# Optimization experiments

Hardware: AMD Instinct MI355X
Metric: run time of the kernel (lower is better)

The kernel has to match this reference:

```python
import jax, jax.numpy as jnp
import numpy as np

N_NODES = 100000
N_EDGES = 3200000
D_IN = 128
D_OUT = 128
EPS = 0.0  # GINConv default eps, not trained


def setup_inputs() -> dict:
    key = jax.random.key(0)
    k1, k2, k3, k4, k5, k6, k7 = jax.random.split(key, 7)
    x = jax.random.normal(k1, (N_NODES, D_IN), dtype=jnp.float32)
    edge_index = jax.random.randint(k2, (2, N_EDGES), 0, N_NODES, dtype=jnp.int64)
    # MLP params: Linear(D_IN->D_OUT), ReLU, Linear(D_OUT->D_OUT)
    s1 = 1.0 / np.sqrt(D_IN)
    s2 = 1.0 / np.sqrt(D_OUT)
    W1 = jax.random.uniform(k3, (D_IN, D_OUT), jnp.float32, -s1, s1)
    b1 = jax.random.uniform(k4, (D_OUT,), jnp.float32, -s1, s1)
    W2 = jax.random.uniform(k5, (D_OUT, D_OUT), jnp.float32, -s2, s2)
    b2 = jax.random.uniform(k6, (D_OUT,), jnp.float32, -s2, s2)
    return {"x": x, "edge_index": edge_index, "W1": W1, "b1": b1, "W2": W2, "b2": b2}


def reference(x, edge_index, W1, b1, W2, b2):
    src, dst = edge_index[0], edge_index[1]
    # message = x[src]; aggregate by sum onto dst (source_to_target flow)
    agg = jax.ops.segment_sum(x[src], dst, num_segments=x.shape[0])  # [N, D_IN]
    h = (1.0 + EPS) * x + agg
    h = jax.nn.relu(h @ W1 + b1)
    return h @ W2 + b2
```

## Files before the change

### kernel.cpp

```cpp
#include <hip/hip_runtime.h>

#define D 128
#define TILE_ROWS 64
#define MLP_THREADS 512
#define SCAN_THREADS 1024
#define BK_NODES 128
#define MAX_BKT 1024
#define EPB 16
#define SC_THREADS 512
#define SC_EPB 24
#define CAPL 6144
#define FMLP_THREADS 512
#define MLP_BM 128
#define HSTR 136

typedef unsigned short ushort_t;
typedef unsigned int uint_t;
typedef __attribute__((ext_vector_type(8))) short short8v;
typedef __attribute__((ext_vector_type(4))) float f32x4;

__device__ __forceinline__ ushort_t f2bf(float f) {
    uint_t u = __float_as_uint(f);
    u = u + 0x7FFFu + ((u >> 16) & 1u);
    return (ushort_t)(u >> 16);
}

__global__ void cast_kernel(const float* __restrict__ x, ushort_t* __restrict__ xh, int n4) {
    int i = blockIdx.x * blockDim.x + threadIdx.x;
    if (i < n4) {
        float4 v = reinterpret_cast<const float4*>(x)[i];
        ushort4 o;
        o.x = f2bf(v.x); o.y = f2bf(v.y); o.z = f2bf(v.z); o.w = f2bf(v.w);
        reinterpret_cast<ushort4*>(xh)[i] = o;
    }
}

__global__ void wprep_kernel(const float* __restrict__ W1, const float* __restrict__ W2,
                             ushort_t* __restrict__ w1t, ushort_t* __restrict__ w2t) {
    int i = blockIdx.x * blockDim.x + threadIdx.x;
    if (i < D * D) {
        int c = i & 127, k = i >> 7;
        w1t[(size_t)c * HSTR + k] = f2bf(W1[(size_t)k * D + c]);
        w2t[(size_t)c * HSTR + k] = f2bf(W2[(size_t)k * D + c]);
    }
}

__global__ void zero_kernel(int* __restrict__ p, int n) {
    int i = blockIdx.x * blockDim.x + threadIdx.x;
    if (i < n) p[i] = 0;
}

__global__ void coarse_hist_kernel(const int* __restrict__ dsts,
                                   int* __restrict__ ghist, int ne, int nbkt) {
    __shared__ int h[MAX_BKT];
    for (int k = threadIdx.x; k < nbkt; k += blockDim.x) h[k] = 0;
    __syncthreads();
    int base = blockIdx.x * blockDim.x * EPB;
    for (int j = 0; j < EPB; ++j) {
        int e = base + j * blockDim.x + threadIdx.x;
        if (e < ne) atomicAdd(&h[dsts[e] >> 7], 1);
    }
    __syncthreads();
    for (int k = threadIdx.x; k < nbkt; k += blockDim.x)
        if (h[k]) atomicAdd(&ghist[k], h[k]);
}

__global__ __launch_bounds__(SCAN_THREADS) void coarse_scan_kernel(
    const int* __restrict__ ghist, int* __restrict__ cbase,
    int* __restrict__ ccursor, int* __restrict__ offsets,
    int nbkt, int nnodes, int ne) {
    __shared__ int sc[SCAN_THREADS];
    int t = threadIdx.x;
    int v = (t < nbkt) ? ghist[t] : 0;
    sc[t] = v;
    __syncthreads();
    for (int off = 1; off < SCAN_THREADS; off <<= 1) {
        int u = (t >= off) ? sc[t - off] : 0;
        __syncthreads();
        sc[t] += u;
        __syncthreads();
    }
    if (t < nbkt) { cbase[t] = sc[t] - v; ccursor[t] = sc[t] - v; }
    if (t == 0) { cbase[nbkt] = sc[SCAN_THREADS - 1]; offsets[nnodes] = ne; }
}

__global__ __launch_bounds__(SC_THREADS) void coarse_scatter_kernel(
    const int* __restrict__ ei, int* __restrict__ ccursor,
    int* __restrict__ pairs, int ne, int nbkt) {
    __shared__ int h[MAX_BKT];
    __shared__ int lbase[MAX_BKT];
    __shared__ int gbase[MAX_BKT];
    __shared__ int lcur[MAX_BKT];
    __shared__ int stot[SC_THREADS];
    __shared__ int stage[SC_THREADS * SC_EPB];

    const int t = threadIdx.x;
    const int base = blockIdx.x * SC_THREADS * SC_EPB;

    for (int k = t; k < MAX_BKT; k += SC_THREADS) h[k] = 0;
    __syncthreads();

    for (int j = 0; j < SC_EPB; ++j) {
        int e = base + j * SC_THREADS + t;
        if (e < ne) atomicAdd(&h[ei[ne + e] >> 7], 1);
    }
    __syncthreads();

    int a0 = h[2 * t], a1 = h[2 * t + 1];
    stot[t] = a0 + a1;
    __syncthreads();
    for (int off = 1; off < SC_THREADS; off <<= 1) {
        int u = (t >= off) ? stot[t - off] : 0;
        __syncthreads();
        stot[t] += u;
        __syncthreads();
    }
    int bexc = stot[t] - (a0 + a1);
    lbase[2 * t] = bexc;
    lbase[2 * t + 1] = bexc + a0;
    lcur[2 * t] = bexc;
    lcur[2 * t + 1] = bexc + a0;
    __syncthreads();

    for (int k = t; k < MAX_BKT; k += SC_THREADS)
        gbase[k] = h[k] ? atomicAdd(&ccursor[k], h[k]) : 0;
    __syncthreads();

    for (int j = 0; j < SC_EPB; ++j) {
        int e = base + j * SC_THREADS + t;
        if (e < ne) {
            int dst = ei[ne + e];
            int src = ei[e];
            int k = dst >> 7;
            int pos = atomicAdd(&lcur[k], 1);
            stage[pos] = (src << 7) | (dst & (BK_NODES - 1));
        }
    }
    __syncthreads();

    const int lane = t & 63, w = t >> 6;
    for (int k = w; k < nbkt; k += (SC_THREADS / 64)) {
        int cnt = h[k];
        int lb = lbase[k], gb = gbase[k];
        for (int i = lane; i < cnt; i += 64)
            pairs[gb + i] = stage[lb + i];
    }
}

__global__ void bucket_csr_kernel(const int* __restrict__ pairs,
                                  const int* __restrict__ cbase,
                                  int* __restrict__ offsets,
                                  int* __restrict__ sorted_src,
                                  int nnodes) {
    __shared__ int h[BK_NODES];
    __shared__ int ex[BK_NODES];
    __shared__ int cur[BK_NODES];
    __shared__ int stage[CAPL];
    int b = blockIdx.x;
    int t = threadIdx.x;
    int rbeg = cbase[b], rend = cbase[b + 1];
    int cnt = rend - rbeg;
    if (t < BK_NODES) h[t] = 0;
    __syncthreads();
    for (int i = rbeg + t; i < rend; i += blockDim.x)
        atomicAdd(&h[pairs[i] & (BK_NODES - 1)], 1);
    __syncthreads();
    if (t < BK_NODES) ex[t] = h[t];
    __syncthreads();
    for (int off = 1; off < BK_NODES; off <<= 1) {
        int u = (t >= off && t < BK_NODES) ? ex[t - off] : 0;
        __syncthreads();
        if (t < BK_NODES) ex[t] += u;
        __syncthreads();
    }
    const bool staged = (cnt <= CAPL);
    if (t < BK_NODES) {
        int e = ex[t] - h[t];
        cur[t] = staged ? e : rbeg + e;
        int node = b * BK_NODES + t;
        if (node < nnodes) offsets[node] = rbeg + e;
    }
    __syncthreads();
    if (staged) {
        for (int i = rbeg + t; i < rend; i += blockDim.x) {
            int p = pairs[i];
            int pos = atomicAdd(&cur[p & (BK_NODES - 1)], 1);
            stage[pos] = p >> 7;
        }
        __syncthreads();
        for (int i = t; i < cnt; i += blockDim.x)
            sorted_src[rbeg + i] = stage[i];
    } else {
        for (int i = rbeg + t; i < rend; i += blockDim.x) {
            int p = pairs[i];
            int pos = atomicAdd(&cur[p & (BK_NODES - 1)], 1);
            sorted_src[pos] = p >> 7;
        }
    }
}

template <int MODE>
__global__ void agg_kernel(const float* __restrict__ x,
                           const ushort_t* __restrict__ xh,
                           const int* __restrict__ sorted_src,
                           const int* __restrict__ offsets,
                           float* __restrict__ out, int nnodes) {
    int gid = blockIdx.x * blockDim.x + threadIdx.x;
    int node = gid >> 6;
    if (node >= nnodes) return;
    int lane = threadIdx.x & 63;
    int beg = offsets[node];
    int end = offsets[node + 1];
    float sx, sy;
    int i = beg;
    if (MODE == 0) {
        const uint_t* xp = reinterpret_cast<const uint_t*>(xh);
        uint_t us = xp[(size_t)node * 64 + lane];
        sx = __uint_as_float(us << 16);
        sy = __uint_as_float(us & 0xffff0000u);
        for (; i + 8 <= end; i += 8) {
            int s0 = sorted_src[i + 0], s1 = sorted_src[i + 1];
            int s2 = sorted_src[i + 2], s3 = sorted_src[i + 3];
            int s4 = sorted_src[i + 4], s5 = sorted_src[i + 5];
            int s6 = sorted_src[i + 6], s7 = sorted_src[i + 7];
            uint_t u0 = xp[(size_t)s0 * 64 + lane];
            uint_t u1 = xp[(size_t)s1 * 64 + lane];
            uint_t u2 = xp[(size_t)s2 * 64 + lane];
            uint_t u3 = xp[(size_t)s3 * 64 + lane];
            uint_t u4 = xp[(size_t)s4 * 64 + lane];
            uint_t u5 = xp[(size_t)s5 * 64 + lane];
            uint_t u6 = xp[(size_t)s6 * 64 + lane];
            uint_t u7 = xp[(size_t)s7 * 64 + lane];
            sx += __uint_as_float(u0 << 16) + __uint_as_float(u1 << 16) +
                  __uint_as_float(u2 << 16) + __uint_as_float(u3 << 16) +
                  __uint_as_float(u4 << 16) + __uint_as_float(u5 << 16) +
                  __uint_as_float(u6 << 16) + __uint_as_float(u7 << 16);
            sy += __uint_as_float(u0 & 0xffff0000u) + __uint_as_float(u1 & 0xffff0000u) +
                  __uint_as_float(u2 & 0xffff0000u) + __uint_as_float(u3 & 0xffff0000u) +
                  __uint_as_float(u4 & 0xffff0000u) + __uint_as_float(u5 & 0xffff0000u) +
                  __uint_as_float(u6 & 0xffff0000u) + __uint_as_float(u7 & 0xffff0000u);
        }
        for (; i < end; ++i) {
            uint_t u = xp[(size_t)sorted_src[i] * 64 + lane];
            sx += __uint_as_float(u << 16);
            sy += __uint_as_float(u & 0xffff0000u);
        }
    } else {
        const float2* xp = reinterpret_cast<const float2*>(x);
        float2 a = xp[(size_t)node * 64 + lane];
        sx = a.x; sy = a.y;
        for (; i + 8 <= end; i += 8) {
            int s0 = sorted_src[i + 0], s1 = sorted_src[i + 1];
            int s2 = sorted_src[i + 2], s3 = sorted_src[i + 3];
            int s4 = sorted_src[i + 4], s5 = sorted_src[i + 5];
            int s6 = sorted_src[i + 6], s7 = sorted_src[i + 7];
            float2 v0 = xp[(size_t)s0 * 64 + lane];
            float2 v1 = xp[(size_t)s1 * 64 + lane];
            float2 v2 = xp[(size_t)s2 * 64 + lane];
            float2 v3 = xp[(size_t)s3 * 64 + lane];
            float2 v4 = xp[(size_t)s4 * 64 + lane];
            float2 v5 = xp[(size_t)s5 * 64 + lane];
            float2 v6 = xp[(size_t)s6 * 64 + lane];
            float2 v7 = xp[(size_t)s7 * 64 + lane];
            sx += ((v0.x + v1.x) + (v2.x + v3.x)) + ((v4.x + v5.x) + (v6.x + v7.x));
            sy += ((v0.y + v1.y) + (v2.y + v3.y)) + ((v4.y + v5.y) + (v6.y + v7.y));
        }
        for (; i < end; ++i) {
            float2 v = xp[(size_t)sorted_src[i] * 64 + lane];
            sx += v.x;
            sy += v.y;
        }
    }
    float2 o;
    o.x = sx;
    o.y = sy;
    reinterpret_cast<float2*>(out)[(size_t)node * 64 + lane] = o;
}

__global__ __launch_bounds__(FMLP_THREADS, 1) void fused_mlp_kernel(
    const float* __restrict__ h, const ushort_t* __restrict__ w1t,
    const ushort_t* __restrict__ w2t, const float* __restrict__ b1,
    const float* __restrict__ b2, float* __restrict__ outp, int nrows) {
    __shared__ ushort_t sh[MLP_BM * HSTR];
    __shared__ ushort_t sw1[D * HSTR];
    __shared__ ushort_t sw2[D * HSTR];
    const int tid = threadIdx.x;
    const int row0 = blockIdx.x * MLP_BM;

    {
        const uint4* s1 = reinterpret_cast<const uint4*>(w1t);
        const uint4* s2 = reinterpret_cast<const uint4*>(w2t);
        uint4* d1 = reinterpret_cast<uint4*>(sw1);
        uint4* d2 = reinterpret_cast<uint4*>(sw2);
        for (int i = tid; i < D * HSTR / 8; i += FMLP_THREADS) { d1[i] = s1[i]; d2[i] = s2[i]; }
    }
    for (int i = tid; i < MLP_BM * 32; i += FMLP_THREADS) {
        int r = i >> 5, c4 = i & 31;
        float4 v = make_float4(0.f, 0.f, 0.f, 0.f);
        if (row0 + r < nrows)
            v = reinterpret_cast<const float4*>(h + (size_t)(row0 + r) * D)[c4];
        ushort4 o;
        o.x = f2bf(v.x); o.y = f2bf(v.y); o.z = f2bf(v.z); o.w = f2bf(v.w);
        *reinterpret_cast<ushort4*>(&sh[r * HSTR + c4 * 4]) = o;
    }
    __syncthreads();

    const int w = tid >> 6, l = tid & 63;
    const int lr = l & 15, lg = l >> 4;
    const int rowb = w * 16;

    short8v A[4];
#pragma unroll
    for (int kk = 0; kk < 4; ++kk)
        A[kk] = *reinterpret_cast<const short8v*>(&sh[(rowb + lr) * HSTR + kk * 32 + lg * 8]);
#pragma unroll
    for (int n = 0; n < 8; ++n) {
        float bv = b1[n * 16 + lr];
        f32x4 acc = {bv, bv, bv, bv};
#pragma unroll
        for (int kk = 0; kk < 4; ++kk) {
            short8v B = *reinterpret_cast<const short8v*>(&sw1[(n * 16 + lr) * HSTR + kk * 32 + lg * 8]);
            acc = __builtin_amdgcn_mfma_f32_16x16x32_bf16(A[kk], B, acc, 0, 0, 0);
        }
#pragma unroll
        for (int r = 0; r < 4; ++r) {
            float v = fmaxf(acc[r], 0.f);
            sh[(rowb + lg * 4 + r) * HSTR + n * 16 + lr] = f2bf(v);
        }
    }

    short8v A2[4];
#pragma unroll
    for (int kk = 0; kk < 4; ++kk)
        A2[kk] = *reinterpret_cast<const short8v*>(&sh[(rowb + lr) * HSTR + kk * 32 + lg * 8]);
#pragma unroll
    for (int n = 0; n < 8; ++n) {
        float bv = b2[n * 16 + lr];
        f32x4 acc = {bv, bv, bv, bv};
#pragma unroll
        for (int kk = 0; kk < 4; ++kk) {
            short8v B = *reinterpret_cast<const short8v*>(&sw2[(n * 16 + lr) * HSTR + kk * 32 + lg * 8]);
            acc = __builtin_amdgcn_mfma_f32_16x16x32_bf16(A2[kk], B, acc, 0, 0, 0);
        }
#pragma unroll
        for (int r = 0; r < 4; ++r) {
            int grow = row0 + rowb + lg * 4 + r;
            if (grow < nrows)
                outp[(size_t)grow * D + n * 16 + lr] = acc[r];
        }
    }
}

__global__ void init_kernel(const float* __restrict__ x, float* __restrict__ out, int n4) {
    int i = blockIdx.x * blockDim.x + threadIdx.x;
    if (i < n4) {
        reinterpret_cast<float4*>(out)[i] = reinterpret_cast<const float4*>(x)[i];
    }
}

__global__ void scatter_kernel(const float* __restrict__ x,
                               const int* __restrict__ ei,
                               float* __restrict__ out, int ne) {
    long long gid = (long long)blockIdx.x * blockDim.x + threadIdx.x;
    int e = (int)(gid >> 5);
    if (e >= ne) return;
    int d0 = ((int)gid & 31) * 4;
    int src = ei[e];
    int dst = ei[ne + e];
    float4 v = *reinterpret_cast<const float4*>(x + (long long)src * D + d0);
    float* o = out + (long long)dst * D + d0;
    atomicAdd(o + 0, v.x);
    atomicAdd(o + 1, v.y);
    atomicAdd(o + 2, v.z);
    atomicAdd(o + 3, v.w);
}

template <bool RELU>
__global__ __launch_bounds__(MLP_THREADS, 1) void mlp_kernel(
    const float* __restrict__ in, const float* __restrict__ W,
    const float* __restrict__ b, float* __restrict__ outp, int nrows) {
    __shared__ float Wl[D][D];
    __shared__ float inl[TILE_ROWS][D + 4];

    const int tid = threadIdx.x;
    const int row0 = blockIdx.x * TILE_ROWS;

    for (int i = tid; i < D * D / 4; i += MLP_THREADS) {
        reinterpret_cast<float4*>(&Wl[0][0])[i] =
            reinterpret_cast<const float4*>(W)[i];
    }
    for (int i = tid; i < TILE_ROWS * (D / 4); i += MLP_THREADS) {
        int r = i >> 5;
        int k4 = i & 31;
        float4 v = make_float4(0.f, 0.f, 0.f, 0.f);
        if (row0 + r < nrows)
            v = *reinterpret_cast<const float4*>(in + (size_t)(row0 + r) * D + 4 * k4);
        *reinterpret_cast<float4*>(&inl[r][4 * k4]) = v;
    }
    __syncthreads();

    const int cg = tid & 31;
    const int rg = tid >> 5;
    const int c0 = cg * 4;
    const int r0 = rg * 4;

    float4 bv = *reinterpret_cast<const float4*>(b + c0);
    float acc[4][4];
#pragma unroll
    for (int i = 0; i < 4; ++i) {
        acc[i][0] = bv.x; acc[i][1] = bv.y; acc[i][2] = bv.z; acc[i][3] = bv.w;
    }

#pragma unroll 4
    for (int k4 = 0; k4 < 32; ++k4) {
        float4 w0 = *reinterpret_cast<const float4*>(&Wl[4 * k4 + 0][c0]);
        float4 w1 = *reinterpret_cast<const float4*>(&Wl[4 * k4 + 1][c0]);
        float4 w2 = *reinterpret_cast<const float4*>(&Wl[4 * k4 + 2][c0]);
        float4 w3 = *reinterpret_cast<const float4*>(&Wl[4 * k4 + 3][c0]);
#pragma unroll
        for (int i = 0; i < 4; ++i) {
            float4 a = *reinterpret_cast<const float4*>(&inl[r0 + i][4 * k4]);
            acc[i][0] += a.x * w0.x + a.y * w1.x + a.z * w2.x + a.w * w3.x;
            acc[i][1] += a.x * w0.y + a.y * w1.y + a.z * w2.y + a.w * w3.y;
            acc[i][2] += a.x * w0.z + a.y * w1.z + a.z * w2.z + a.w * w3.z;
            acc[i][3] += a.x * w0.w + a.y * w1.w + a.z * w2.w + a.w * w3.w;
        }
    }

#pragma unroll
    for (int i = 0; i < 4; ++i) {
        int r = row0 + r0 + i;
        if (r < nrows) {
            float4 o;
            if (RELU) {
                o.x = fmaxf(acc[i][0], 0.f); o.y = fmaxf(acc[i][1], 0.f);
                o.z = fmaxf(acc[i][2], 0.f); o.w = fmaxf(acc[i][3], 0.f);
            } else {
                o.x = acc[i][0]; o.y = acc[i][1]; o.z = acc[i][2]; o.w = acc[i][3];
            }
            *reinterpret_cast<float4*>(outp + (size_t)r * D + c0) = o;
        }
    }
}

extern "C" void kernel_launch(void* const* d_in, const int* in_sizes, int n_in,
                              void* d_out, int out_size, void* d_ws, size_t ws_size,
                              hipStream_t stream) {
    const float* x = (const float*)d_in[0];
    const int* ei = (const int*)d_in[1];
    const float* W1 = (const float*)d_in[2];
    const float* b1 = (const float*)d_in[3];
    const float* W2 = (const float*)d_in[4];
    const float* b2 = (const float*)d_in[5];
    float* out = (float*)d_out;

    const int nrows = in_sizes[0] / D;
    const int ne = in_sizes[1] / 2;
    const int nbkt = (nrows + BK_NODES - 1) / BK_NODES;

    size_t xh_bytes = (((size_t)nrows * D * sizeof(ushort_t)) + 15) & ~(size_t)15;
    size_t csr_bytes = ((size_t)(nrows + 1) + 2 * (size_t)ne + 3 * (size_t)nbkt + 1) * sizeof(int);
    size_t need_fp = csr_bytes;
    size_t need_bf = xh_bytes + csr_bytes;
    size_t wt_bytes = (size_t)D * HSTR * sizeof(ushort_t);
    size_t wt_off = (need_bf + 15) & ~(size_t)15;
    size_t need_mfma = wt_off + 2 * wt_bytes;

    const int hblocks = (ne + 256 * EPB - 1) / (256 * EPB);
    const int sblocks2 = (ne + SC_THREADS * SC_EPB - 1) / (SC_THREADS * SC_EPB);

    bool use_mfma = false;
    ushort_t* w1t = nullptr;
    ushort_t* w2t = nullptr;

    if (nbkt <= MAX_BKT && ws_size >= need_fp) {
        const bool bf = (ws_size >= need_bf);
        use_mfma = (ws_size >= need_mfma);
        char* wp = (char*)d_ws;
        ushort_t* xh = nullptr;
        if (bf) { xh = (ushort_t*)wp; wp += xh_bytes; }
        int* offsets = (int*)wp;
        int* sorted_src = offsets + (nrows + 1);
        int* pairs = sorted_src + ne;
        int* ghist = pairs + ne;
        int* cbase = ghist + nbkt;
        int* ccursor = cbase + (nbkt + 1);
        if (use_mfma) {
            w1t = (ushort_t*)((char*)d_ws + wt_off);
            w2t = (ushort_t*)((char*)d_ws + wt_off + wt_bytes);
        }

        if (bf) {
            int n4 = nrows * (D / 4);
            cast_kernel<<<(n4 + 255) / 256, 256, 0, stream>>>(x, xh, n4);
        }
        if (use_mfma)
            wprep_kernel<<<(D * D + 255) / 256, 256, 0, stream>>>(W1, W2, w1t, w2t);
        zero_kernel<<<(nbkt + 255) / 256, 256, 0, stream>>>(ghist, nbkt);
        coarse_hist_kernel<<<hblocks, 256, 0, stream>>>(ei + ne, ghist, ne, nbkt);
        coarse_scan_kernel<<<1, SCAN_THREADS, 0, stream>>>(ghist, cbase, ccursor,
                                                           offsets, nbkt, nrows, ne);
        coarse_scatter_kernel<<<sblocks2, SC_THREADS, 0, stream>>>(ei, ccursor, pairs, ne, nbkt);
        bucket_csr_kernel<<<nbkt, 256, 0, stream>>>(pairs, cbase, offsets, sorted_src, nrows);

        long long athreads = (long long)nrows * 64;
        int ablocks = (int)((athreads + 255) / 256);
        if (bf)
            agg_kernel<0><<<ablocks, 256, 0, stream>>>(x, xh, sorted_src, offsets, out, nrows);
        else
            agg_kernel<1><<<ablocks, 256, 0, stream>>>(x, nullptr, sorted_src, offsets, out, nrows);
    } else {
        int n4 = nrows * (D / 4);
        init_kernel<<<(n4 + 255) / 256, 256, 0, stream>>>(x, out, n4);
        long long sthreads = (long long)ne * 32;
        scatter_kernel<<<(int)((sthreads + 255) / 256), 256, 0, stream>>>(x, ei, out, ne);
    }

    if (use_mfma) {
        int fblocks = (nrows + MLP_BM - 1) / MLP_BM;
        fused_mlp_kernel<<<fblocks, FMLP_THREADS, 0, stream>>>(out, w1t, w2t, b1, b2, out, nrows);
    } else {
        int mblocks = (nrows + TILE_ROWS - 1) / TILE_ROWS;
        mlp_kernel<true><<<mblocks, MLP_THREADS, 0, stream>>>(out, W1, b1, out, nrows);
        mlp_kernel<false><<<mblocks, MLP_THREADS, 0, stream>>>(out, W2, b2, out, nrows);
    }
}
```

Measured before the change: 254.0 us.

## Write aggregated features as bf16 and split wave into two half-edge streams

```diff
diff --git a/kernel.cpp b/kernel.cpp
--- a/kernel.cpp
+++ b/kernel.cpp
@@ -24,6 +24,8 @@
     u = u + 0x7FFFu + ((u >> 16) & 1u);
     return (ushort_t)(u >> 16);
 }
+__device__ __forceinline__ float bf_lo(uint_t u) { return __uint_as_float(u << 16); }
+__device__ __forceinline__ float bf_hi(uint_t u) { return __uint_as_float(u & 0xffff0000u); }
 
 __global__ void cast_kernel(const float* __restrict__ x, ushort_t* __restrict__ xh, int n4) {
     int i = blockIdx.x * blockDim.x + threadIdx.x;
@@ -199,88 +201,122 @@
     }
 }
 
-template <int MODE>
-__global__ void agg_kernel(const float* __restrict__ x,
-                           const ushort_t* __restrict__ xh,
-                           const int* __restrict__ sorted_src,
-                           const int* __restrict__ offsets,
-                           float* __restrict__ out, int nnodes) {
+__global__ void agg_bf_kernel(const ushort_t* __restrict__ xh,
+                              const int* __restrict__ sorted_src,
+                              const int* __restrict__ offsets,
+                              float* __restrict__ out,
+                              uint_t* __restrict__ hbf, int nnodes) {
+    int gid = blockIdx.x * blockDim.x + threadIdx.x;
+    int node = gid >> 6;
+    if (node >= nnodes) return;
+    const int lane = threadIdx.x & 63;
+    const int col = lane & 31;
+    const int half = lane >> 5;
+    const uint2* xp = reinterpret_cast<const uint2*>(xh);
+    int beg = offsets[node];
+    int end = offsets[node + 1];
+
+    float s0, s1, s2, s3;
+    {
+        uint2 u = xp[(size_t)node * 32 + col];
+        if (half) { u.x = 0u; u.y = 0u; }
+        s0 = bf_lo(u.x); s1 = bf_hi(u.x);
+        s2 = bf_lo(u.y); s3 = bf_hi(u.y);
+    }
+
+    int i = beg;
+    for (; i + 16 <= end; i += 16) {
+        uint2 v0 = xp[(size_t)sorted_src[i + 0 + half] * 32 + col];
+        uint2 v1 = xp[(size_t)sorted_src[i + 2 + half] * 32 + col];
+        uint2 v2 = xp[(size_t)sorted_src[i + 4 + half] * 32 + col];
+        uint2 v3 = xp[(size_t)sorted_src[i + 6 + half] * 32 + col];
+        uint2 v4 = xp[(size_t)sorted_src[i + 8 + half] * 32 + col];
+        uint2 v5 = xp[(size_t)sorted_src[i + 10 + half] * 32 + col];
+        uint2 v6 = xp[(size_t)sorted_src[i + 12 + half] * 32 + col];
+        uint2 v7 = xp[(size_t)sorted_src[i + 14 + half] * 32 + col];
+        s0 += bf_lo(v0.x) + bf_lo(v1.x) + bf_lo(v2.x) + bf_lo(v3.x) +
+              bf_lo(v4.x) + bf_lo(v5.x) + bf_lo(v6.x) + bf_lo(v7.x);
+        s1 += bf_hi(v0.x) + bf_hi(v1.x) + bf_hi(v2.x) + bf_hi(v3.x) +
+              bf_hi(v4.x) + bf_hi(v5.x) + bf_hi(v6.x) + bf_hi(v7.x);
+        s2 += bf_lo(v0.y) + bf_lo(v1.y) + bf_lo(v2.y) + bf_lo(v3.y) +
+              bf_lo(v4.y) + bf_lo(v5.y) + bf_lo(v6.y) + bf_lo(v7.y);
+        s3 += bf_hi(v0.y) + bf_hi(v1.y) + bf_hi(v2.y) + bf_hi(v3.y) +
+              bf_hi(v4.y) + bf_hi(v5.y) + bf_hi(v6.y) + bf_hi(v7.y);
+    }
+    for (; i + 2 <= end; i += 2) {
+        uint2 u = xp[(size_t)sorted_src[i + half] * 32 + col];
+        s0 += bf_lo(u.x); s1 += bf_hi(u.x);
+        s2 += bf_lo(u.y); s3 += bf_hi(u.y);
+    }
+    if (i < end && half == 0) {
+        uint2 u = xp[(size_t)sorted_src[i] * 32 + col];
+        s0 += bf_lo(u.x); s1 += bf_hi(u.x);
+        s2 += bf_lo(u.y); s3 += bf_hi(u.y);
+    }
+
+    s0 += __shfl_xor(s0, 32);
+    s1 += __shfl_xor(s1, 32);
+    s2 += __shfl_xor(s2, 32);
+    s3 += __shfl_xor(s3, 32);
+
+    if (half == 0) {
+        if (hbf) {
+            uint_t lo = (uint_t)f2bf(s0) | ((uint_t)f2bf(s1) << 16);
+            uint_t hi = (uint_t)f2bf(s2) | ((uint_t)f2bf(s3) << 16);
+            uint2 o; o.x = lo; o.y = hi;
+            reinterpret_cast<uint2*>(hbf)[(size_t)node * 32 + col] = o;
+        } else {
+            float4 o; o.x = s0; o.y = s1; o.z = s2; o.w = s3;
+            reinterpret_cast<float4*>(out + (size_t)node * D)[col] = o;
+        }
+    }
+}
+
+__global__ void agg_fp_kernel(const float* __restrict__ x,
+                              const int* __restrict__ sorted_src,
+                              const int* __restrict__ offsets,
+                              float* __restrict__ out, int nnodes) {
     int gid = blockIdx.x * blockDim.x + threadIdx.x;
     int node = gid >> 6;
     if (node >= nnodes) return;
     int lane = threadIdx.x & 63;
     int beg = offsets[node];
     int end = offsets[node + 1];
-    float sx, sy;
+    const float2* xp = reinterpret_cast<const float2*>(x);
+    float2 a = xp[(size_t)node * 64 + lane];
+    float sx = a.x, sy = a.y;
     int i = beg;
-    if (MODE == 0) {
-        const uint_t* xp = reinterpret_cast<const uint_t*>(xh);
-        uint_t us = xp[(size_t)node * 64 + lane];
-        sx = __uint_as_float(us << 16);
-        sy = __uint_as_float(us & 0xffff0000u);
-        for (; i + 8 <= end; i += 8) {
-            int s0 = sorted_src[i + 0], s1 = sorted_src[i + 1];
-            int s2 = sorted_src[i + 2], s3 = sorted_src[i + 3];
-            int s4 = sorted_src[i + 4], s5 = sorted_src[i + 5];
-            int s6 = sorted_src[i + 6], s7 = sorted_src[i + 7];
-            uint_t u0 = xp[(size_t)s0 * 64 + lane];
-            uint_t u1 = xp[(size_t)s1 * 64 + lane];
-            uint_t u2 = xp[(size_t)s2 * 64 + lane];
-            uint_t u3 = xp[(size_t)s3 * 64 + lane];
-            uint_t u4 = xp[(size_t)s4 * 64 + lane];
-            uint_t u5 = xp[(size_t)s5 * 64 + lane];
-            uint_t u6 = xp[(size_t)s6 * 64 + lane];
-            uint_t u7 = xp[(size_t)s7 * 64 + lane];
-            sx += __uint_as_float(u0 << 16) + __uint_as_float(u1 << 16) +
-                  __uint_as_float(u2 << 16) + __uint_as_float(u3 << 16) +
-                  __uint_as_float(u4 << 16) + __uint_as_float(u5 << 16) +
-                  __uint_as_float(u6 << 16) + __uint_as_float(u7 << 16);
-            sy += __uint_as_float(u0 & 0xffff0000u) + __uint_as_float(u1 & 0xffff0000u) +
-                  __uint_as_float(u2 & 0xffff0000u) + __uint_as_float(u3 & 0xffff0000u) +
-                  __uint_as_float(u4 & 0xffff0000u) + __uint_as_float(u5 & 0xffff0000u) +
-                  __uint_as_float(u6 & 0xffff0000u) + __uint_as_float(u7 & 0xffff0000u);
-        }
-        for (; i < end; ++i) {
-            uint_t u = xp[(size_t)sorted_src[i] * 64 + lane];
-            sx += __uint_as_float(u << 16);
-            sy += __uint_as_float(u & 0xffff0000u);
-        }
-    } else {
-        const float2* xp = reinterpret_cast<const float2*>(x);
-        float2 a = xp[(size_t)node * 64 + lane];
-        sx = a.x; sy = a.y;
-        for (; i + 8 <= end; i += 8) {
-            int s0 = sorted_src[i + 0], s1 = sorted_src[i + 1];
-            int s2 = sorted_src[i + 2], s3 = sorted_src[i + 3];
-            int s4 = sorted_src[i + 4], s5 = sorted_src[i + 5];
-            int s6 = sorted_src[i + 6], s7 = sorted_src[i + 7];
-            float2 v0 = xp[(size_t)s0 * 64 + lane];
-            float2 v1 = xp[(size_t)s1 * 64 + lane];
-            float2 v2 = xp[(size_t)s2 * 64 + lane];
-            float2 v3 = xp[(size_t)s3 * 64 + lane];
-            float2 v4 = xp[(size_t)s4 * 64 + lane];
-            float2 v5 = xp[(size_t)s5 * 64 + lane];
-            float2 v6 = xp[(size_t)s6 * 64 + lane];
-            float2 v7 = xp[(size_t)s7 * 64 + lane];
-            sx += ((v0.x + v1.x) + (v2.x + v3.x)) + ((v4.x + v5.x) + (v6.x + v7.x));
-            sy += ((v0.y + v1.y) + (v2.y + v3.y)) + ((v4.y + v5.y) + (v6.y + v7.y));
-        }
-        for (; i < end; ++i) {
-            float2 v = xp[(size_t)sorted_src[i] * 64 + lane];
-            sx += v.x;
-            sy += v.y;
-        }
-    }
-    float2 o;
-    o.x = sx;
-    o.y = sy;
+    for (; i + 8 <= end; i += 8) {
+        int s0 = sorted_src[i + 0], s1 = sorted_src[i + 1];
+        int s2 = sorted_src[i + 2], s3 = sorted_src[i + 3];
+        int s4 = sorted_src[i + 4], s5 = sorted_src[i + 5];
+        int s6 = sorted_src[i + 6], s7 = sorted_src[i + 7];
+        float2 v0 = xp[(size_t)s0 * 64 + lane];
+        float2 v1 = xp[(size_t)s1 * 64 + lane];
+        float2 v2 = xp[(size_t)s2 * 64 + lane];
+        float2 v3 = xp[(size_t)s3 * 64 + lane];
+        float2 v4 = xp[(size_t)s4 * 64 + lane];
+        float2 v5 = xp[(size_t)s5 * 64 + lane];
+        float2 v6 = xp[(size_t)s6 * 64 + lane];
+        float2 v7 = xp[(size_t)s7 * 64 + lane];
+        sx += ((v0.x + v1.x) + (v2.x + v3.x)) + ((v4.x + v5.x) + (v6.x + v7.x));
+        sy += ((v0.y + v1.y) + (v2.y + v3.y)) + ((v4.y + v5.y) + (v6.y + v7.y));
+    }
+    for (; i < end; ++i) {
+        float2 v = xp[(size_t)sorted_src[i] * 64 + lane];
+        sx += v.x;
+        sy += v.y;
+    }
+    float2 o; o.x = sx; o.y = sy;
     reinterpret_cast<float2*>(out)[(size_t)node * 64 + lane] = o;
 }
 
+template <bool BF>
 __global__ __launch_bounds__(FMLP_THREADS, 1) void fused_mlp_kernel(
-    const float* __restrict__ h, const ushort_t* __restrict__ w1t,
-    const ushort_t* __restrict__ w2t, const float* __restrict__ b1,
-    const float* __restrict__ b2, float* __restrict__ outp, int nrows) {
+    const float* __restrict__ h, const uint_t* __restrict__ hbf,
+    const ushort_t* __restrict__ w1t, const ushort_t* __restrict__ w2t,
+    const float* __restrict__ b1, const float* __restrict__ b2,
+    float* __restrict__ outp, int nrows) {
     __shared__ ushort_t sh[MLP_BM * HSTR];
     __shared__ ushort_t sw1[D * HSTR];
     __shared__ ushort_t sw2[D * HSTR];
@@ -294,14 +330,24 @@
         uint4* d2 = reinterpret_cast<uint4*>(sw2);
         for (int i = tid; i < D * HSTR / 8; i += FMLP_THREADS) { d1[i] = s1[i]; d2[i] = s2[i]; }
     }
-    for (int i = tid; i < MLP_BM * 32; i += FMLP_THREADS) {
-        int r = i >> 5, c4 = i & 31;
-        float4 v = make_float4(0.f, 0.f, 0.f, 0.f);
-        if (row0 + r < nrows)
-            v = reinterpret_cast<const float4*>(h + (size_t)(row0 + r) * D)[c4];
-        ushort4 o;
-        o.x = f2bf(v.x); o.y = f2bf(v.y); o.z = f2bf(v.z); o.w = f2bf(v.w);
-        *reinterpret_cast<ushort4*>(&sh[r * HSTR + c4 * 4]) = o;
+    if (BF) {
+        for (int i = tid; i < MLP_BM * 16; i += FMLP_THREADS) {
+            int r = i >> 4, c = i & 15;
+            uint4 v = make_uint4(0u, 0u, 0u, 0u);
+            if (row0 + r < nrows)
+                v = reinterpret_cast<const uint4*>(hbf + (size_t)(row0 + r) * 64)[c];
+            *reinterpret_cast<uint4*>(&sh[r * HSTR + c * 8]) = v;
+        }
+    } else {
+        for (int i = tid; i < MLP_BM * 32; i += FMLP_THREADS) {
+            int r = i >> 5, c4 = i & 31;
+            float4 v = make_float4(0.f, 0.f, 0.f, 0.f);
+            if (row0 + r < nrows)
+                v = reinterpret_cast<const float4*>(h + (size_t)(row0 + r) * D)[c4];
+            ushort4 o;
+            o.x = f2bf(v.x); o.y = f2bf(v.y); o.z = f2bf(v.z); o.w = f2bf(v.w);
+            *reinterpret_cast<ushort4*>(&sh[r * HSTR + c4 * 4]) = o;
+        }
     }
     __syncthreads();
 
@@ -465,17 +511,23 @@
     size_t wt_bytes = (size_t)D * HSTR * sizeof(ushort_t);
     size_t wt_off = (need_bf + 15) & ~(size_t)15;
     size_t need_mfma = wt_off + 2 * wt_bytes;
+    size_t hbf_off = (need_mfma + 15) & ~(size_t)15;
+    size_t hbf_bytes = (size_t)nrows * D * sizeof(ushort_t);
+    size_t need_hbf = hbf_off + hbf_bytes;
 
     const int hblocks = (ne + 256 * EPB - 1) / (256 * EPB);
     const int sblocks2 = (ne + SC_THREADS * SC_EPB - 1) / (SC_THREADS * SC_EPB);
 
     bool use_mfma = false;
+    bool use_hbf = false;
     ushort_t* w1t = nullptr;
     ushort_t* w2t = nullptr;
+    uint_t* hbf = nullptr;
 
     if (nbkt <= MAX_BKT && ws_size >= need_fp) {
         const bool bf = (ws_size >= need_bf);
         use_mfma = (ws_size >= need_mfma);
+        use_hbf = bf && use_mfma && (ws_size >= need_hbf);
         char* wp = (char*)d_ws;
         ushort_t* xh = nullptr;
         if (bf) { xh = (ushort_t*)wp; wp += xh_bytes; }
@@ -489,6 +541,7 @@
             w1t = (ushort_t*)((char*)d_ws + wt_off);
             w2t = (ushort_t*)((char*)d_ws + wt_off + wt_bytes);
         }
+        if (use_hbf) hbf = (uint_t*)((char*)d_ws + hbf_off);
 
         if (bf) {
             int n4 = nrows * (D / 4);
@@ -506,9 +559,9 @@
         long long athreads = (long long)nrows * 64;
         int ablocks = (int)((athreads + 255) / 256);
         if (bf)
-            agg_kernel<0><<<ablocks, 256, 0, stream>>>(x, xh, sorted_src, offsets, out, nrows);
+            agg_bf_kernel<<<ablocks, 256, 0, stream>>>(xh, sorted_src, offsets, out, hbf, nrows);
         else
-            agg_kernel<1><<<ablocks, 256, 0, stream>>>(x, nullptr, sorted_src, offsets, out, nrows);
+            agg_fp_kernel<<<ablocks, 256, 0, stream>>>(x, sorted_src, offsets, out, nrows);
     } else {
         int n4 = nrows * (D / 4);
         init_kernel<<<(n4 + 255) / 256, 256, 0, stream>>>(x, out, n4);
@@ -518,7 +571,12 @@
 
     if (use_mfma) {
         int fblocks = (nrows + MLP_BM - 1) / MLP_BM;
-        fused_mlp_kernel<<<fblocks, FMLP_THREADS, 0, stream>>>(out, w1t, w2t, b1, b2, out, nrows);
+        if (use_hbf)
+            fused_mlp_kernel<true><<<fblocks, FMLP_THREADS, 0, stream>>>(
+                out, hbf, w1t, w2t, b1, b2, out, nrows);
+        else
+            fused_mlp_kernel<false><<<fblocks, FMLP_THREADS, 0, stream>>>(
+                out, nullptr, w1t, w2t, b1, b2, out, nrows);
     } else {
         int mblocks = (nrows + TILE_ROWS - 1) / TILE_ROWS;
         mlp_kernel<true><<<mblocks, MLP_THREADS, 0, stream>>>(out, W1, b1, out, nrows);
```

Result: faster. 244.6 us (-3.7%).
